# Optimization experiments

Measured on AMD Instinct MI355X. Metric: run time of the kernel, lower is better.

Reference implementation:

```python
import jax, jax.numpy as jnp
import numpy as np
from jax.ops import segment_sum, segment_max

B, NPG, EPG = 2048, 32, 64          # graphs per drug, nodes/graph, edges/graph
N, E = B * NPG, B * EPG
FIN, EIN = 70, 6
HID, H, C = 128, 2, 64              # hidd_dim, conv heads, head_out_feats
NBLK, NCLASS = 4, 2
CAH, CAD = 8, 128                   # co-attention heads, dim_head


def _elu(x):
    return jnp.where(x > 0, x, jnp.expm1(x))


def _ln_graph(x, batch, w, b):
    # PyG LayerNorm(mode='graph'): normalize over all nodes+channels of each graph.
    cnt = jnp.float32(NPG * x.shape[1])  # all graphs have NPG nodes
    mean = segment_sum(x.sum(-1), batch, num_segments=B) / cnt
    xc = x - mean[batch][:, None]
    var = segment_sum((xc * xc).sum(-1), batch, num_segments=B) / cnt
    return xc * jax.lax.rsqrt(var + 1e-5)[batch][:, None] * w + b


def _ln(x, w, b):
    mu = x.mean(-1, keepdims=True)
    v = ((x - mu) ** 2).mean(-1, keepdims=True)
    return (x - mu) * jax.lax.rsqrt(v + 1e-5) * w + b


def _tconv(x, src, dst, ea, Wq, bq, Wk, bk, Wv, bv, We, Ws, bs):
    # PyG TransformerConv: edge-attention gather -> softmax over incoming edges -> scatter.
    q = (x @ Wq + bq).reshape(-1, H, C)
    k = (x @ Wk + bk).reshape(-1, H, C)
    v = (x @ Wv + bv).reshape(-1, H, C)
    e = (ea @ We).reshape(-1, H, C)
    kj = k[src] + e                                   # [E,H,C]
    a = (q[dst] * kj).sum(-1) * (C ** -0.5)           # [E,H]
    amax = segment_max(a, dst, num_segments=N)
    a = jnp.exp(a - amax[dst])
    a = a / (segment_sum(a, dst, num_segments=N)[dst] + 1e-16)
    out = segment_sum((v[src] + e) * a[:, :, None], dst, num_segments=N)
    return out.reshape(-1, H * C) + x @ Ws + bs       # root/skip connection


def _pool(x, src, dst, ea, batch, ebatch, w_rel, b_rel, w_root, W_re, b_re):
    # SAGPooling(min_score=-1): GraphConv score, per-graph softmax, all nodes kept,
    # then score-weighted global_add_pool; edge_attr pooled per graph and merged.
    agg = segment_sum(x[src], dst, num_segments=N)    # GraphConv 'add' aggregation
    score = agg @ w_rel + b_rel + x @ w_root          # [N]
    smax = segment_max(score, batch, num_segments=B)
    sexp = jnp.exp(score - smax[batch])
    score = sexp / (segment_sum(sexp, batch, num_segments=B)[batch] + 1e-16)
    g = segment_sum(x * score[:, None], batch, num_segments=B)      # [B,HID]
    ge = _elu(segment_sum(ea, ebatch, num_segments=B) @ W_re + b_re)
    g = g * ge
    return g / jnp.maximum(jnp.linalg.norm(g, axis=1, keepdims=True), 1e-12)


def _coattn(qx, kvx, lw, lb, Wq, Wkv, Wo):
    qx = _ln(qx, lw, lb)
    kvx = _ln(kvx, lw, lb)
    b, n = qx.shape[0], qx.shape[1]
    q = (qx @ Wq).reshape(b, n, CAH, CAD).transpose(0, 2, 1, 3)
    k, v = jnp.split(kvx @ Wkv, 2, axis=-1)
    k = k.reshape(b, n, CAH, CAD).transpose(0, 2, 1, 3)
    v = v.reshape(b, n, CAH, CAD).transpose(0, 2, 1, 3)
    attn = jax.nn.softmax(jnp.einsum('bhnd,bhmd->bhnm', q, k) * (CAD ** -0.5), axis=-1)
    o = jnp.einsum('bhnm,bhmd->bhnd', attn, v).transpose(0, 2, 1, 3).reshape(b, n, CAH * CAD)
    return o @ Wo


def setup_inputs() -> dict:
    key = jax.random.key(0)
    ks = iter(jax.random.split(key, 64))

    def nrm(shape, fan):
        return jax.random.normal(next(ks), shape, jnp.float32) * (fan ** -0.5)

    inp = {}
    inp['x1'] = jax.random.normal(next(ks), (N, FIN), jnp.float32)
    inp['x2'] = jax.random.normal(next(ks), (N, FIN), jnp.float32)
    inp['ea1'] = jax.random.normal(next(ks), (E, EIN), jnp.float32)
    inp['ea2'] = jax.random.normal(next(ks), (E, EIN), jnp.float32)
    inp['W_node'] = nrm((FIN, HID), FIN); inp['b_node'] = jnp.zeros((HID,), jnp.float32)
    inp['W_edge'] = nrm((EIN, 64), EIN); inp['b_edge'] = jnp.zeros((64,), jnp.float32)
    inp['ln0_w'] = jnp.ones((HID,), jnp.float32); inp['ln0_b'] = jnp.zeros((HID,), jnp.float32)
    inp['Wq'] = nrm((NBLK, 2, HID, HID), HID); inp['bq'] = jnp.zeros((NBLK, 2, HID), jnp.float32)
    inp['Wk'] = nrm((NBLK, 2, HID, HID), HID); inp['bk'] = jnp.zeros((NBLK, 2, HID), jnp.float32)
    inp['Wv'] = nrm((NBLK, 2, HID, HID), HID); inp['bv'] = jnp.zeros((NBLK, 2, HID), jnp.float32)
    inp['We'] = nrm((NBLK, 2, 64, HID), 64)
    inp['Ws'] = nrm((NBLK, 2, HID, HID), HID); inp['bs'] = jnp.zeros((NBLK, 2, HID), jnp.float32)
    inp['Wup'] = nrm((NBLK, 2, 64, 64), 64); inp['bup'] = jnp.zeros((NBLK, 2, 64), jnp.float32)
    inp['lnw'] = jnp.ones((NBLK, 2, HID), jnp.float32); inp['lnb'] = jnp.zeros((NBLK, 2, HID), jnp.float32)
    inp['w_rel'] = nrm((HID,), HID); inp['b_rel'] = jnp.zeros((), jnp.float32)
    inp['w_root'] = nrm((HID,), HID)
    inp['W_re'] = nrm((64, HID), 64); inp['b_re'] = jnp.zeros((HID,), jnp.float32)
    inp['ca_lw'] = jnp.ones((HID,), jnp.float32); inp['ca_lb'] = jnp.zeros((HID,), jnp.float32)
    inp['Wq_ca'] = nrm((HID, CAH * CAD), HID)
    inp['Wkv_ca'] = nrm((HID, 2 * CAH * CAD), HID)
    inp['Wo_ca'] = nrm((CAH * CAD, HID), CAH * CAD)
    inp['W_merge'] = nrm((NBLK * NBLK, NCLASS), NBLK * NBLK)
    inp['b_merge'] = jnp.zeros((NCLASS,), jnp.float32)
    off = jnp.repeat(jnp.arange(B, dtype=jnp.int32) * NPG, EPG)
    inp['edge_index1'] = jax.random.randint(next(ks), (2, E), 0, NPG, jnp.int32) + off[None, :]
    inp['edge_index2'] = jax.random.randint(next(ks), (2, E), 0, NPG, jnp.int32) + off[None, :]
    inp['batch1'] = jnp.repeat(jnp.arange(B, dtype=jnp.int32), NPG)
    inp['batch2'] = jnp.repeat(jnp.arange(B, dtype=jnp.int32), NPG)
    inp['ebatch1'] = jnp.repeat(jnp.arange(B, dtype=jnp.int32), EPG)
    inp['ebatch2'] = jnp.repeat(jnp.arange(B, dtype=jnp.int32), EPG)
    return inp


def reference(x1, x2, ea1, ea2, W_node, b_node, W_edge, b_edge, ln0_w, ln0_b,
              Wq, bq, Wk, bk, Wv, bv, We, Ws, bs, Wup, bup, lnw, lnb,
              w_rel, b_rel, w_root, W_re, b_re, ca_lw, ca_lb, Wq_ca, Wkv_ca, Wo_ca,
              W_merge, b_merge, edge_index1, edge_index2, batch1, batch2, ebatch1, ebatch2):
    s1, d1 = edge_index1[0], edge_index1[1]
    s2, d2 = edge_index2[0], edge_index2[1]
    x1 = _elu(_ln_graph(x1 @ W_node + b_node, batch1, ln0_w, ln0_b))
    x2 = _elu(_ln_graph(x2 @ W_node + b_node, batch2, ln0_w, ln0_b))
    ea1 = _elu(ea1 @ W_edge + b_edge)
    ea2 = _elu(ea2 @ W_edge + b_edge)

    def block(i, x, ea, src, dst, batch):
        x = _tconv(x, src, dst, ea, Wq[i, 0], bq[i, 0], Wk[i, 0], bk[i, 0],
                   Wv[i, 0], bv[i, 0], We[i, 0], Ws[i, 0], bs[i, 0])
        x = _elu(_ln_graph(x, batch, lnw[i, 0], lnb[i, 0]))
        ea = _elu(ea @ Wup[i, 0] + bup[i, 0])
        x = _tconv(x, src, dst, ea, Wq[i, 1], bq[i, 1], Wk[i, 1], bk[i, 1],
                   Wv[i, 1], bv[i, 1], We[i, 1], Ws[i, 1], bs[i, 1])
        ea_next = ea @ Wup[i, 1] + bup[i, 1]
        x = _elu(_ln_graph(x, batch, lnw[i, 1], lnb[i, 1]))
        return x, _elu(ea_next)

    hs, ts = [], []
    for i in range(NBLK):
        x1, ea1 = block(i, x1, ea1, s1, d1, batch1)
        x2, ea2 = block(i, x2, ea2, s2, d2, batch2)
        hs.append(_pool(x1, s1, d1, ea1, batch1, ebatch1, w_rel, b_rel, w_root, W_re, b_re))
        ts.append(_pool(x2, s2, d2, ea2, batch2, ebatch2, w_rel, b_rel, w_root, W_re, b_re))
    rh = jnp.stack(hs, 1)  # [B, NBLK, HID]
    rt = jnp.stack(ts, 1)
    ha = _coattn(rh, rt, ca_lw, ca_lb, Wq_ca, Wkv_ca, Wo_ca)
    ta = _coattn(rt, rh, ca_lw, ca_lb, Wq_ca, Wkv_ca, Wo_ca)
    m = jnp.einsum('bnd,bmd->bnm', ha, ta).reshape(ha.shape[0], NBLK * NBLK)
    return jax.nn.softmax(m @ W_merge + b_merge, axis=-1)
```

## Files before the change

### kernel.cpp

```cpp
#include <hip/hip_runtime.h>
#include <cstddef>
#include <cstdint>

#define NGRAPH 2048
#define NPG    32
#define EPG    64
#define NNODE  (NGRAPH*NPG)
#define NEDGE  (NGRAPH*EPG)
#define FINDIM 70
#define EINDIM 6
#define HID    128
#define NBLK   4
#define CAH    8
#define CAD    128
#define ES     68
#define XS     132

typedef __attribute__((ext_vector_type(8))) short bf16x8_t;
typedef __attribute__((ext_vector_type(4))) float f32x4;
typedef unsigned short ushortb;

#define MF3(accv, Ah_, Al_, Bh_, Bl_)                                          \
  accv = __builtin_amdgcn_mfma_f32_16x16x32_bf16(Ah_, Bh_, accv, 0, 0, 0);     \
  accv = __builtin_amdgcn_mfma_f32_16x16x32_bf16(Ah_, Bl_, accv, 0, 0, 0);     \
  accv = __builtin_amdgcn_mfma_f32_16x16x32_bf16(Al_, Bh_, accv, 0, 0, 0);

__device__ inline void split8(const float* p, bf16x8_t& h, bf16x8_t& l) {
  float4 v0 = *(const float4*)p, v1 = *(const float4*)(p + 4);
  float vv[8] = {v0.x, v0.y, v0.z, v0.w, v1.x, v1.y, v1.z, v1.w};
#pragma unroll
  for (int j = 0; j < 8; j++) {
    unsigned u = __builtin_bit_cast(unsigned, vv[j]);
    h[j] = (short)(u >> 16);
    float r = vv[j] - __builtin_bit_cast(float, u & 0xFFFF0000u);
    l[j] = (short)(__builtin_bit_cast(unsigned, r) >> 16);
  }
}

template<bool BIAS, bool ELU>
__global__ __launch_bounds__(256) void gemm_kernel(
    const float* __restrict__ A, const float* __restrict__ W,
    const float* __restrict__ bias, float* __restrict__ C,
    int M, int K, int Nc) {
  __shared__ float As[8][64];
  __shared__ float Bs[8][65];
  const int bm = blockIdx.y * 64, bn = blockIdx.x * 64;
  const int tid = threadIdx.x;
  const int tr = tid >> 4, tc = tid & 15;
  float acc[4][4];
#pragma unroll
  for (int i = 0; i < 4; i++)
#pragma unroll
    for (int j = 0; j < 4; j++) acc[i][j] = 0.f;
  for (int k0 = 0; k0 < K; k0 += 8) {
#pragma unroll
    for (int l = 0; l < 2; l++) {
      int idx = tid + l * 256;
      int r = idx >> 3, c = idx & 7;
      As[c][r] = (k0 + c < K) ? A[(size_t)(bm + r) * K + k0 + c] : 0.f;
      int rw = idx >> 6, cw = idx & 63;
      Bs[rw][cw] = (k0 + rw < K) ? W[(size_t)(k0 + rw) * Nc + bn + cw] : 0.f;
    }
    __syncthreads();
#pragma unroll
    for (int kk = 0; kk < 8; kk++) {
      float a_[4], w_[4];
#pragma unroll
      for (int i = 0; i < 4; i++) a_[i] = As[kk][tr * 4 + i];
#pragma unroll
// ... 122 lines not shown
  for (int m = 0; m < 2; m++)
#pragma unroll
    for (int n = 0; n < 4; n++) {
      int col = bn + wc * 64 + n * 16 + l16;
#pragma unroll
      for (int r = 0; r < 4; r++) {
        int row = bm + wr * 32 + m * 16 + lk * 4 + r;
        C[(size_t)row * N + col] = acc[m][n][r];
      }
    }
}

static void run_mf8(const float* A, const ushortb* Wh, const ushortb* Wl,
                    float* C, int M, int K, int N, hipStream_t st) {
  dim3 grid(N / 128, M / 128), block(512);
  gemm_mfma8_kernel<<<grid, block, 0, st>>>(A, Wh, Wl, C, M, K, N);
}

__global__ void ln_graph_elu_kernel(const float* __restrict__ in, float* __restrict__ out,
                                    const float* __restrict__ w, const float* __restrict__ b) {
  const int g = blockIdx.x, t = threadIdx.x;
  const float* xg = in + (size_t)g * NPG * HID;
  float* og = out + (size_t)g * NPG * HID;
  float vals[16];
  float s = 0.f, ss = 0.f;
#pragma unroll
  for (int i = 0; i < 16; i++) {
    float v = xg[t + i * 256];
    vals[i] = v; s += v; ss += v * v;
  }
  __shared__ float ws0[4], ws1[4];
  for (int off = 32; off > 0; off >>= 1) { s += __shfl_down(s, off); ss += __shfl_down(ss, off); }
  int wid = t >> 6, lane = t & 63;
  if (lane == 0) { ws0[wid] = s; ws1[wid] = ss; }
  __syncthreads();
  if (t == 0) {
    float S = 0.f, SS = 0.f;
    for (int i = 0; i < 4; i++) { S += ws0[i]; SS += ws1[i]; }
    float mean = S / 4096.f;
    float var = SS / 4096.f - mean * mean;
    ws0[0] = mean; ws1[0] = rsqrtf(var + 1e-5f);
  }
  __syncthreads();
  float mean = ws0[0], inv = ws1[0];
#pragma unroll
  for (int i = 0; i < 16; i++) {
    int idx = t + i * 256;
    int ch = idx & 127;
    float y = (vals[i] - mean) * inv * w[ch] + b[ch];
    og[idx] = y > 0.f ? y : expm1f(y);
  }
}

template<bool POOL>
__global__ __launch_bounds__(256, 4) void mega_kernel(
    float* __restrict__ xb, float* __restrict__ ea,
    const ushortb* __restrict__ Wqkvh, const ushortb* __restrict__ Wqkvl,
    const ushortb* __restrict__ Wsh, const ushortb* __restrict__ Wsl,
    const ushortb* __restrict__ WeTh, const ushortb* __restrict__ WeTl,
    const ushortb* __restrict__ Wuph, const ushortb* __restrict__ Wupl,
    const float* __restrict__ bqkv_, const float* __restrict__ bs_,
    const float* __restrict__ bup_, const float* __restrict__ lnw_,
    const float* __restrict__ lnb_,
    const float* __restrict__ w_rel, const float* __restrict__ b_rel,
    const float* __restrict__ w_root, const float* __restrict__ W_re,
    const float* __restrict__ b_re, float* __restrict__ outp, int blk,
    const int* __restrict__ src, const int* __restrict__ dst) {
  const int g = blockIdx.x, t = threadIdx.x;
  const int lane = t & 63, w = t >> 6, l16 = lane & 15, lk = lane >> 4;
  __shared__ float el[EPG * ES];
  __shared__ float qs2[NPG * ES];
  __shared__ float ks2[NPG * ES];
  __shared__ unsigned char lists[NPG * EPG];
  __shared__ int deg_[NPG];
  __shared__ int sl[EPG], dl[EPG];
  __shared__ float alE[128];
  __shared__ float red0[NPG], red1[NPG];

  if (t < EPG) { sl[t] = src[g * EPG + t] - g * NPG; dl[t] = dst[g * EPG + t] - g * NPG; }
  if (t < NPG) {
    int c = 0;
    for (int e = 0; e < EPG; e++)
      if (dl[e] == t) lists[t * EPG + (c++)] = (unsigned char)e;
    deg_[t] = c;
  }

  bf16x8_t xh[2][4], xL[2][4];
#pragma unroll
  for (int m = 0; m < 2; m++)
#pragma unroll
    for (int kc = 0; kc < 4; kc++)
      split8(xb + ((size_t)g * NPG + m * 16 + l16) * HID + kc * 32 + lk * 8,
             xh[m][kc], xL[m][kc]);
  const float* eag = ea + ((size_t)g * EPG + w * 16 + l16) * 64;

  float accH0[8], accH1[8];
#pragma unroll
  for (int c = 0; c < 8; c++) { accH0[c] = 0.f; accH1[c] = 0.f; }

  auto proj = [&](int baseN, float* dstL) {
    f32x4 pa0 = (f32x4)0.f, pa1 = (f32x4)0.f;
#pragma unroll
    for (int kc = 0; kc < 4; kc++) {
      size_t o = (size_t)(baseN + w * 16 + l16) * HID + kc * 32 + lk * 8;
      bf16x8_t bh = *(const bf16x8_t*)(Wqkvh + o);
      bf16x8_t bl = *(const bf16x8_t*)(Wqkvl + o);
      MF3(pa0, xh[0][kc], xL[0][kc], bh, bl);
      MF3(pa1, xh[1][kc], xL[1][kc], bh, bl);
    }
    float bv = bqkv_[baseN + w * 16 + l16];
#pragma unroll
    for (int r = 0; r < 4; r++) {
      dstL[(lk * 4 + r) * ES + w * 16 + l16] = pa0[r] + bv;
      dstL[(16 + lk * 4 + r) * ES + w * 16 + l16] = pa1[r] + bv;
    }
  };

  auto head = [&](const int h, float (&acc8)[8]) {
    {
      bf16x8_t ea0h, ea0l, ea1h, ea1l;
      split8(eag + lk * 8, ea0h, ea0l);
      split8(eag + 32 + lk * 8, ea1h, ea1l);
#pragma unroll 1
      for (int n = 0; n < 4; n++) {
        f32x4 acc = (f32x4)0.f;
        size_t o0 = (size_t)(h * 64 + n * 16 + l16) * 64 + lk * 8;
        bf16x8_t bh0 = *(const bf16x8_t*)(WeTh + o0);
        bf16x8_t bl0 = *(const bf16x8_t*)(WeTl + o0);
        MF3(acc, ea0h, ea0l, bh0, bl0);
        bf16x8_t bh1 = *(const bf16x8_t*)(WeTh + o0 + 32);
        bf16x8_t bl1 = *(const bf16x8_t*)(WeTl + o0 + 32);
        MF3(acc, ea1h, ea1l, bh1, bl1);
#pragma unroll
        for (int r = 0; r < 4; r++)
          el[(w * 16 + lk * 4 + r) * ES + n * 16 + l16] = acc[r];
      }
    }
    proj(h * 64, qs2);
    proj(128 + h * 64, ks2);
    __syncthreads();
    {
      const int e2 = t >> 2, part = t & 3;
      const float* qp = qs2 + dl[e2] * ES + part * 16;
      const float* kp = ks2 + sl[e2] * ES + part * 16;
      const float* ep = el + e2 * ES + part * 16;
      float s = 0.f;
#pragma unroll
      for (int c = 0; c < 16; c += 4) {
        float4 qv = *(const float4*)(qp + c);
        float4 kv = *(const float4*)(kp + c);
        float4 ev = *(const float4*)(ep + c);
        s += qv.x * (kv.x + ev.x) + qv.y * (kv.y + ev.y) +
             qv.z * (kv.z + ev.z) + qv.w * (kv.w + ev.w);
      }
      s += __shfl_xor(s, 1);
      s += __shfl_xor(s, 2);
      if (part == 0) alE[e2] = s * 0.125f;
    }
    __syncthreads();
    {
      const int n = t >> 3, part = t & 7;
      float m = -1e30f;
#pragma unroll 1
      for (int i = 0; i < 8; i++) {
        int e2 = part * 8 + i;
        if (dl[e2] == n) m = fmaxf(m, alE[e2]);
      }
      m = fmaxf(m, __shfl_xor(m, 1));
      m = fmaxf(m, __shfl_xor(m, 2));
      m = fmaxf(m, __shfl_xor(m, 4));
      float su = 0.f;
#pragma unroll 1
      for (int i = 0; i < 8; i++) {
        int e2 = part * 8 + i;
        if (dl[e2] == n) su += expf(alE[e2] - m);
      }
      su += __shfl_xor(su, 1);
      su += __shfl_xor(su, 2);
      su += __shfl_xor(su, 4);
      if (part == 0) { red0[n] = m; red1[n] = su; }
    }
    __syncthreads();
    if (t < EPG) {
      int n = dl[t];
      alE[t] = expf(alE[t] - red0[n]) / (red1[n] + 1e-16f);
    }
    f32x4 va0 = (f32x4)0.f, va1 = (f32x4)0.f;
#pragma unroll
    for (int kc = 0; kc < 4; kc++) {
      size_t o = (size_t)(256 + h * 64 + w * 16 + l16) * HID + kc * 32 + lk * 8;
      bf16x8_t bh = *(const bf16x8_t*)(Wqkvh + o);
      bf16x8_t bl = *(const bf16x8_t*)(Wqkvl + o);
      MF3(va0, xh[0][kc], xL[0][kc], bh, bl);
      MF3(va1, xh[1][kc], xL[1][kc], bh, bl);
    }
    float bv = bqkv_[256 + h * 64 + w * 16 + l16];
    __syncthreads();
#pragma unroll
    for (int r = 0; r < 4; r++) {
      ks2[(lk * 4 + r) * ES + w * 16 + l16] = va0[r] + bv;
      ks2[(16 + lk * 4 + r) * ES + w * 16 + l16] = va1[r] + bv;
    }
    __syncthreads();
    {
      const int n = t >> 3, cg = t & 7;
      const int dg = deg_[n];
      for (int i = 0; i < dg; i++) {
        const int e2 = lists[n * EPG + i];
        const float a = alE[e2];
        const float* vp = ks2 + sl[e2] * ES + cg * 8;
        const float* ep = el + e2 * ES + cg * 8;
        float4 v0 = *(const float4*)vp, v1 = *(const float4*)(vp + 4);
        float4 e0 = *(const float4*)ep, e1 = *(const float4*)(ep + 4);
        acc8[0] += a * (v0.x + e0.x); acc8[1] += a * (v0.y + e0.y);
        acc8[2] += a * (v0.z + e0.z); acc8[3] += a * (v0.w + e0.w);
        acc8[4] += a * (v1.x + e1.x); acc8[5] += a * (v1.y + e1.y);
        acc8[6] += a * (v1.z + e1.z); acc8[7] += a * (v1.w + e1.w);
      }
    }
    __syncthreads();
  };

  head(0, accH0);
  head(1, accH1);

  {
#pragma unroll
    for (int n = 0; n < 2; n++) {
      f32x4 sa0 = (f32x4)0.f, sa1 = (f32x4)0.f;
#pragma unroll
      for (int kc = 0; kc < 4; kc++) {
        size_t o = (size_t)(w * 32 + n * 16 + l16) * HID + kc * 32 + lk * 8;
        bf16x8_t bh = *(const bf16x8_t*)(Wsh + o);
        bf16x8_t bl = *(const bf16x8_t*)(Wsl + o);
        MF3(sa0, xh[0][kc], xL[0][kc], bh, bl);
        MF3(sa1, xh[1][kc], xL[1][kc], bh, bl);
      }
      int col = w * 32 + n * 16 + l16;
      float bv = bs_[col];
#pragma unroll
      for (int r = 0; r < 4; r++) {
        el[(lk * 4 + r) * XS + col] = sa0[r] + bv;
        el[(16 + lk * 4 + r) * XS + col] = sa1[r] + bv;
      }
    }
  }
  f32x4 ua[4];
  {
    bf16x8_t ea0h, ea0l, ea1h, ea1l;
    split8(eag + lk * 8, ea0h, ea0l);
    split8(eag + 32 + lk * 8, ea1h, ea1l);
#pragma unroll
    for (int n = 0; n < 4; n++) {
      f32x4 acc = (f32x4)0.f;
      size_t o0 = (size_t)(n * 16 + l16) * 64 + lk * 8;
      bf16x8_t bh0 = *(const bf16x8_t*)(Wuph + o0);
      bf16x8_t bl0 = *(const bf16x8_t*)(Wupl + o0);
      MF3(acc, ea0h, ea0l, bh0, bl0);
      bf16x8_t bh1 = *(const bf16x8_t*)(Wuph + o0 + 32);
      bf16x8_t bl1 = *(const bf16x8_t*)(Wupl + o0 + 32);
      MF3(acc, ea1h, ea1l, bh1, bl1);
      int col = n * 16 + l16;
      float bv = bup_[col];
#pragma unroll
      for (int r = 0; r < 4; r++) {
        float y = acc[r] + bv;
        y = y > 0.f ? y : expm1f(y);
        ua[n][r] = y;
        ea[((size_t)g * EPG + w * 16 + lk * 4 + r) * 64 + col] = y;
      }
    }
  }
  __syncthreads();
  {
    const int n = t >> 3, cg = t & 7;
    float v16[16];
#pragma unroll
    for (int c = 0; c < 8; c++) {
      v16[c] = accH0[c] + el[n * XS + cg * 8 + c];
      v16[8 + c] = accH1[c] + el[n * XS + 64 + cg * 8 + c];
    }
    float s = 0.f, ss = 0.f;
#pragma unroll
    for (int j = 0; j < 16; j++) { s += v16[j]; ss += v16[j] * v16[j]; }
    for (int o2 = 32; o2 > 0; o2 >>= 1) { s += __shfl_down(s, o2); ss += __shfl_down(ss, o2); }
    if (lane == 0) { red0[w] = s; red1[w] = ss; }
    __syncthreads();
    if (t == 0) {
      float S = red0[0] + red0[1] + red0[2] + red0[3];
      float SS = red1[0] + red1[1] + red1[2] + red1[3];
      float mean = S / 4096.f;
      float var = SS / 4096.f - mean * mean;
      red0[0] = mean; red1[0] = rsqrtf(var + 1e-5f);
    }
    __syncthreads();
    float mean = red0[0], inv = red1[0];
    float* xg = xb + (size_t)g * NPG * HID;
#pragma unroll
    for (int hh = 0; hh < 2; hh++)
#pragma unroll
      for (int c = 0; c < 8; c++) {
        int col = hh * 64 + cg * 8 + c;
        float y = (v16[hh * 8 + c] - mean) * inv * lnw_[col] + lnb_[col];
        y = y > 0.f ? y : expm1f(y);
        xg[n * HID + col] = y;
        el[n * XS + col] = y;
      }
  }

  if constexpr (POOL) {
    __syncthreads();
    {
#pragma unroll
      for (int n = 0; n < 4; n++) {
        float s = ua[n][0] + ua[n][1] + ua[n][2] + ua[n][3];
        s += __shfl_xor(s, 16);
        s += __shfl_xor(s, 32);
        if (lk == 0) qs2[w * 64 + n * 16 + l16] = s;
      }
      const int n = t >> 3, part = t & 7;
      float s = 0.f;
      for (int c = part * 16; c < part * 16 + 16; c++)
        s += el[n * XS + c] * w_root[c];
      const int dg = deg_[n];
      for (int i = 0; i < dg; i++) {
        int sn = sl[lists[n * EPG + i]];
        for (int c = part * 16; c < part * 16 + 16; c++)
          s += el[sn * XS + c] * w_rel[c];
      }
      s += __shfl_xor(s, 1);
      s += __shfl_xor(s, 2);
      s += __shfl_xor(s, 4);
      if (part == 0) alE[n] = s + b_rel[0];
    }
    __syncthreads();
    if (t < 64)
      alE[64 + t] = qs2[t] + qs2[64 + t] + qs2[128 + t] + qs2[192 + t];
    if (t >= 128 && t < 160) {
      int n = t - 128;
      float sc = alE[n];
      float m = sc;
      for (int o2 = 1; o2 <= 16; o2 <<= 1) m = fmaxf(m, __shfl_xor(m, o2));
      float e = expf(sc - m);
      float su = e;
      for (int o2 = 1; o2 <= 16; o2 <<= 1) su += __shfl_xor(su, o2);
      alE[n] = e / (su + 1e-16f);
    }
    __syncthreads();
    if (t < HID) {
      const int ch = t;
      float gv = 0.f;
      for (int n = 0; n < NPG; n++) gv += alE[n] * el[n * XS + ch];
      float s2 = b_re[ch];
      for (int k2 = 0; k2 < 64; k2++) s2 += alE[64 + k2] * W_re[k2 * HID + ch];
      s2 = s2 > 0.f ? s2 : expm1f(s2);
      float gl = gv * s2;
      qs2[256 + ch] = gl;
      float sq = gl * gl;
      for (int o2 = 32; o2 > 0; o2 >>= 1) sq += __shfl_down(sq, o2);
      if (lane == 0) red0[w] = sq;
    }
    __syncthreads();
    if (t == 0) red1[0] = fmaxf(sqrtf(red0[0] + red0[1]), 1e-12f);
    __syncthreads();
    if (t < HID)
      outp[((size_t)g * NBLK + blk) * HID + t] = qs2[256 + t] / red1[0];
  }
}

__global__ void ln_row_kernel(const float* __restrict__ in, float* __restrict__ out,
                              const float* __restrict__ w, const float* __restrict__ b) {
  const int r = blockIdx.x, t = threadIdx.x;
  float v = in[(size_t)r * HID + t];
  float s = v, ss = v * v;
  for (int off = 32; off > 0; off >>= 1) { s += __shfl_down(s, off); ss += __shfl_down(ss, off); }
  __shared__ float s0[2], s1[2];
  if ((t & 63) == 0) { s0[t >> 6] = s; s1[t >> 6] = ss; }
  __syncthreads();
  float S = s0[0] + s0[1], SS = s1[0] + s1[1];
  float mean = S / 128.f, var = SS / 128.f - mean * mean;
  out[(size_t)r * HID + t] = (v - mean) * rsqrtf(var + 1e-5f) * w[t] + b[t];
}

__global__ void coattn_kernel(const float* __restrict__ qb, const float* __restrict__ kvb,
                              float* __restrict__ ob) {
  const int bh = blockIdx.x, b = bh >> 3, h = bh & 7, t = threadIdx.x;
  __shared__ float attn[4][4];
  __shared__ float red[64];
  const int pair = t >> 2, part = t & 3;
  const int n = pair >> 2, m = pair & 3;
  const float* qp = qb + ((size_t)(b * 4 + n) * (CAH * CAD)) + h * CAD;
  const float* kp = kvb + ((size_t)(b * 4 + m) * (2 * CAH * CAD)) + h * CAD;
  float s = 0.f;
  for (int d = part * 32; d < part * 32 + 32; d++) s += qp[d] * kp[d];
  red[t] = s;
  __syncthreads();
  if (t < 16) {
    float sc = (red[t * 4] + red[t * 4 + 1] + red[t * 4 + 2] + red[t * 4 + 3]) * 0.08838834764831845f;
    attn[t >> 2][t & 3] = sc;
  }
  __syncthreads();
  if (t < 4) {
    float m_ = -1e30f;
    for (int j = 0; j < 4; j++) m_ = fmaxf(m_, attn[t][j]);
    float ex[4], su = 0.f;
    for (int j = 0; j < 4; j++) { ex[j] = expf(attn[t][j] - m_); su += ex[j]; }
    for (int j = 0; j < 4; j++) attn[t][j] = ex[j] / su;
  }
  __syncthreads();
  for (int i = t; i < 512; i += 64) {
    int n2 = i >> 7, d = i & 127;
    float acc = 0.f;
    for (int m2 = 0; m2 < 4; m2++)
      acc += attn[n2][m2] * kvb[((size_t)(b * 4 + m2) * (2 * CAH * CAD)) + CAH * CAD + h * CAD + d];
    ob[((size_t)(b * 4 + n2) * (CAH * CAD)) + h * CAD + d] = acc;
  }
}

__global__ void final_kernel(const float* __restrict__ ha, const float* __restrict__ ta,
// ... 68 lines not shown
    off += ((elems * 4 + 255) & ~(size_t)255);
    return r;
  };
  auto allocb = [&](size_t elems) {
    ushortb* r = (ushortb*)(base + off);
    off += ((elems * 2 + 255) & ~(size_t)255);
    return r;
  };
  float* xb  = alloc((size_t)NNODE * HID);
  float* ea  = alloc((size_t)NEDGE * 64);
  float* big = alloc((size_t)8192 * 2048);
  float* hs  = alloc((size_t)NGRAPH * NBLK * HID);
  float* ts  = alloc((size_t)NGRAPH * NBLK * HID);
  float* rhn = alloc((size_t)NGRAPH * NBLK * HID);
  float* rtn = alloc((size_t)NGRAPH * NBLK * HID);
  float* hab = alloc((size_t)NGRAPH * NBLK * HID);
  float* tab = alloc((size_t)NGRAPH * NBLK * HID);
  ushortb* Wqkvh = allocb((size_t)8 * 384 * 128); ushortb* Wqkvl = allocb((size_t)8 * 384 * 128);
  ushortb* Wsh = allocb(8 * 16384);  ushortb* Wsl = allocb(8 * 16384);
  ushortb* Wuph = allocb(8 * 4096);  ushortb* Wupl = allocb(8 * 4096);
  ushortb* WeTh = allocb(8 * 8192);  ushortb* WeTl = allocb(8 * 8192);
  ushortb* Wqcah = allocb(131072);   ushortb* Wqcal = allocb(131072);
  ushortb* Wkvh = allocb(262144);    ushortb* Wkvl = allocb(262144);
  ushortb* Woh = allocb(131072);     ushortb* Wol = allocb(131072);
  float* bqkv = alloc(8 * 384);
  if (off > ws_size) return;

  float* qc  = xb;
  float* kvc = big;
  float* oc  = ea;

  auto convw = [&](const float* s, ushortb* h, ushortb* l, int K, int N, int B,
                   int dstN, int nOff) {
    int tot = B * K * N;
    convw_kernel<<<(tot + 255) / 256, 256, 0, stream>>>(s, h, l, K, N, tot, dstN, nOff);
  };
  convw(Wq, Wqkvh, Wqkvl, 128, 128, 8, 384, 0);
  convw(Wk, Wqkvh, Wqkvl, 128, 128, 8, 384, 128);
  convw(Wv, Wqkvh, Wqkvl, 128, 128, 8, 384, 256);
  convw(Wskip, Wsh, Wsl, 128, 128, 8, 128, 0);
  convw(Wup, Wuph, Wupl, 64, 64, 8, 64, 0);
  convw(We, WeTh, WeTl, 64, 128, 8, 128, 0);
  convw(Wq_ca, Wqcah, Wqcal, 128, 1024, 1, 1024, 0);
  convw(Wkv_ca, Wkvh, Wkvl, 128, 2048, 1, 2048, 0);
  convw(Wo_ca, Woh, Wol, 1024, 128, 1, 128, 0);
  bcat_kernel<<<(8 * 384 + 255) / 256, 256, 0, stream>>>(bq, bk, bv, bqkv);

  for (int d2 = 0; d2 < 2; ++d2) {
    const int* src = ei[d2];
    const int* dst = ei[d2] + NEDGE;
    run_gemm(xin[d2], W_node, b_node, xb, NNODE, FINDIM, HID, false, stream);
    ln_graph_elu_kernel<<<NGRAPH, 256, 0, stream>>>(xb, xb, ln0_w, ln0_b);
    run_gemm(eain[d2], W_edge, b_edge, ea, NEDGE, EINDIM, 64, true, stream);
    float* outp = d2 == 0 ? hs : ts;
    for (int i = 0; i < NBLK; ++i) {
      int pi0 = i * 2, pi1 = i * 2 + 1;
      mega_kernel<false><<<NGRAPH, 256, 0, stream>>>(
          xb, ea,
          Wqkvh + (size_t)pi0 * 49152, Wqkvl + (size_t)pi0 * 49152,
          Wsh + (size_t)pi0 * 16384, Wsl + (size_t)pi0 * 16384,
          WeTh + (size_t)pi0 * 8192, WeTl + (size_t)pi0 * 8192,
          Wuph + (size_t)pi0 * 4096, Wupl + (size_t)pi0 * 4096,
          bqkv + pi0 * 384, bs + pi0 * 128, bup + pi0 * 64,
          lnw + pi0 * 128, lnb + pi0 * 128,
          w_rel, b_rel, w_root, W_re, b_re, nullptr, 0, src, dst);
      mega_kernel<true><<<NGRAPH, 256, 0, stream>>>(
          xb, ea,
          Wqkvh + (size_t)pi1 * 49152, Wqkvl + (size_t)pi1 * 49152,
          Wsh + (size_t)pi1 * 16384, Wsl + (size_t)pi1 * 16384,
          WeTh + (size_t)pi1 * 8192, WeTl + (size_t)pi1 * 8192,
          Wuph + (size_t)pi1 * 4096, Wupl + (size_t)pi1 * 4096,
          bqkv + pi1 * 384, bs + pi1 * 128, bup + pi1 * 64,
          lnw + pi1 * 128, lnb + pi1 * 128,
          w_rel, b_rel, w_root, W_re, b_re, outp, i, src, dst);
    }
  }

  ln_row_kernel<<<NGRAPH * NBLK, 128, 0, stream>>>(hs, rhn, ca_lw, ca_lb);
  ln_row_kernel<<<NGRAPH * NBLK, 128, 0, stream>>>(ts, rtn, ca_lw, ca_lb);
  run_mf8(rhn, Wqcah, Wqcal, qc, NGRAPH * NBLK, 128, 1024, stream);
  run_mf8(rtn, Wkvh, Wkvl, kvc, NGRAPH * NBLK, 128, 2048, stream);
  coattn_kernel<<<NGRAPH * CAH, 64, 0, stream>>>(qc, kvc, oc);
  run_mf8(oc, Woh, Wol, hab, NGRAPH * NBLK, 1024, 128, stream);
  run_mf8(rtn, Wqcah, Wqcal, qc, NGRAPH * NBLK, 128, 1024, stream);
  run_mf8(rhn, Wkvh, Wkvl, kvc, NGRAPH * NBLK, 128, 2048, stream);
  coattn_kernel<<<NGRAPH * CAH, 64, 0, stream>>>(qc, kvc, oc);
  run_mf8(oc, Woh, Wol, tab, NGRAPH * NBLK, 1024, 128, stream);

  final_kernel<<<NGRAPH, 64, 0, stream>>>(hab, tab, W_merge, b_merge, out);
}
```

Baseline: 3.239 ms.

## Fuse all eight conv layers into one persistent per-graph kernel with on-chip state

Replaces eight separate per-layer launches with one kernel per drug that loops over all conv layers. Node features and edge attributes stay in shared memory and registers between layers instead of going through global memory. This removes launch overhead and the global traffic to write and re-read x and ea each layer. The cost is a longer kernel body, some shared-memory aliasing (qks reused for edge attributes), and possible register pressure that could lower occupancy.

```diff
diff --git a/kernel.cpp b/kernel.cpp
--- a/kernel.cpp
+++ b/kernel.cpp
@@ -15,6 +15,7 @@
 #define CAD    128
 #define ES     68
 #define XS     132
+#define TS     66
 
 typedef __attribute__((ext_vector_type(8))) short bf16x8_t;
 typedef __attribute__((ext_vector_type(4))) float f32x4;
@@ -243,30 +244,30 @@
   }
 }
 
-template<bool POOL>
 __global__ __launch_bounds__(256, 4) void mega_kernel(
-    float* __restrict__ xb, float* __restrict__ ea,
-    const ushortb* __restrict__ Wqkvh, const ushortb* __restrict__ Wqkvl,
-    const ushortb* __restrict__ Wsh, const ushortb* __restrict__ Wsl,
-    const ushortb* __restrict__ WeTh, const ushortb* __restrict__ WeTl,
-    const ushortb* __restrict__ Wuph, const ushortb* __restrict__ Wupl,
-    const float* __restrict__ bqkv_, const float* __restrict__ bs_,
-    const float* __restrict__ bup_, const float* __restrict__ lnw_,
-    const float* __restrict__ lnb_,
+    const float* __restrict__ xb, const float* __restrict__ ea,
+    const ushortb* __restrict__ Wqkvh_, const ushortb* __restrict__ Wqkvl_,
+    const ushortb* __restrict__ Wsh_, const ushortb* __restrict__ Wsl_,
+    const ushortb* __restrict__ WeTh_, const ushortb* __restrict__ WeTl_,
+    const ushortb* __restrict__ Wuph_, const ushortb* __restrict__ Wupl_,
+    const float* __restrict__ bqkvA, const float* __restrict__ bsA,
+    const float* __restrict__ bupA, const float* __restrict__ lnwA,
+    const float* __restrict__ lnbA,
     const float* __restrict__ w_rel, const float* __restrict__ b_rel,
     const float* __restrict__ w_root, const float* __restrict__ W_re,
-    const float* __restrict__ b_re, float* __restrict__ outp, int blk,
+    const float* __restrict__ b_re, float* __restrict__ outp,
     const int* __restrict__ src, const int* __restrict__ dst) {
   const int g = blockIdx.x, t = threadIdx.x;
   const int lane = t & 63, w = t >> 6, l16 = lane & 15, lk = lane >> 4;
   __shared__ float el[EPG * ES];
-  __shared__ float qs2[NPG * ES];
-  __shared__ float ks2[NPG * ES];
+  __shared__ float qks[2 * NPG * ES];
   __shared__ unsigned char lists[NPG * EPG];
   __shared__ int deg_[NPG];
   __shared__ int sl[EPG], dl[EPG];
   __shared__ float alE[128];
   __shared__ float red0[NPG], red1[NPG];
+  float* qs2 = qks;
+  float* ks2 = qks + NPG * ES;
 
   if (t < EPG) { sl[t] = src[g * EPG + t] - g * NPG; dl[t] = dst[g * EPG + t] - g * NPG; }
   if (t < NPG) {
@@ -283,279 +284,299 @@
     for (int kc = 0; kc < 4; kc++)
       split8(xb + ((size_t)g * NPG + m * 16 + l16) * HID + kc * 32 + lk * 8,
              xh[m][kc], xL[m][kc]);
-  const float* eag = ea + ((size_t)g * EPG + w * 16 + l16) * 64;
-
-  float accH0[8], accH1[8];
-#pragma unroll
-  for (int c = 0; c < 8; c++) { accH0[c] = 0.f; accH1[c] = 0.f; }
-
-  auto proj = [&](int baseN, float* dstL) {
-    f32x4 pa0 = (f32x4)0.f, pa1 = (f32x4)0.f;
-#pragma unroll
-    for (int kc = 0; kc < 4; kc++) {
-      size_t o = (size_t)(baseN + w * 16 + l16) * HID + kc * 32 + lk * 8;
-      bf16x8_t bh = *(const bf16x8_t*)(Wqkvh + o);
-      bf16x8_t bl = *(const bf16x8_t*)(Wqkvl + o);
-      MF3(pa0, xh[0][kc], xL[0][kc], bh, bl);
-      MF3(pa1, xh[1][kc], xL[1][kc], bh, bl);
-    }
-    float bv = bqkv_[baseN + w * 16 + l16];
-#pragma unroll
-    for (int r = 0; r < 4; r++) {
-      dstL[(lk * 4 + r) * ES + w * 16 + l16] = pa0[r] + bv;
-      dstL[(16 + lk * 4 + r) * ES + w * 16 + l16] = pa1[r] + bv;
-    }
-  };
-
-  auto head = [&](const int h, float (&acc8)[8]) {
+  bf16x8_t eah[2], eaL[2];
+  {
+    const float* eag = ea + ((size_t)g * EPG + w * 16 + l16) * 64;
+    split8(eag + lk * 8, eah[0], eaL[0]);
+    split8(eag + 32 + lk * 8, eah[1], eaL[1]);
+  }
+
+  for (int pi = 0; pi < 8; ++pi) {
+    const ushortb* Wqkvh = Wqkvh_ + (size_t)pi * 49152;
+    const ushortb* Wqkvl = Wqkvl_ + (size_t)pi * 49152;
+    const ushortb* Wsh = Wsh_ + (size_t)pi * 16384;
+    const ushortb* Wsl = Wsl_ + (size_t)pi * 16384;
+    const ushortb* WeTh = WeTh_ + (size_t)pi * 8192;
+    const ushortb* WeTl = WeTl_ + (size_t)pi * 8192;
+    const ushortb* Wuph = Wuph_ + (size_t)pi * 4096;
+    const ushortb* Wupl = Wupl_ + (size_t)pi * 4096;
+    const float* bqkv_ = bqkvA + pi * 384;
+    const float* bs_ = bsA + pi * 128;
+    const float* bup_ = bupA + pi * 64;
+    const float* lnw_ = lnwA + pi * 128;
+    const float* lnb_ = lnbA + pi * 128;
+
+    float accH0[8], accH1[8];
+#pragma unroll
+    for (int c = 0; c < 8; c++) { accH0[c] = 0.f; accH1[c] = 0.f; }
+
+    auto proj = [&](int baseN, float* dstL) {
+      f32x4 pa0 = (f32x4)0.f, pa1 = (f32x4)0.f;
+#pragma unroll
+      for (int kc = 0; kc < 4; kc++) {
+        size_t o = (size_t)(baseN + w * 16 + l16) * HID + kc * 32 + lk * 8;
+        bf16x8_t bh = *(const bf16x8_t*)(Wqkvh + o);
+        bf16x8_t bl = *(const bf16x8_t*)(Wqkvl + o);
+        MF3(pa0, xh[0][kc], xL[0][kc], bh, bl);
+        MF3(pa1, xh[1][kc], xL[1][kc], bh, bl);
+      }
+      float bv = bqkv_[baseN + w * 16 + l16];
+#pragma unroll
+      for (int r = 0; r < 4; r++) {
+        dstL[(lk * 4 + r) * ES + w * 16 + l16] = pa0[r] + bv;
+        dstL[(16 + lk * 4 + r) * ES + w * 16 + l16] = pa1[r] + bv;
+      }
+    };
+
+    auto head = [&](const int h, float (&acc8)[8]) {
+      {
+#pragma unroll 1
+        for (int n = 0; n < 4; n++) {
+          f32x4 acc = (f32x4)0.f;
+          size_t o0 = (size_t)(h * 64 + n * 16 + l16) * 64 + lk * 8;
+          bf16x8_t bh0 = *(const bf16x8_t*)(WeTh + o0);
+          bf16x8_t bl0 = *(const bf16x8_t*)(WeTl + o0);
+          MF3(acc, eah[0], eaL[0], bh0, bl0);
+          bf16x8_t bh1 = *(const bf16x8_t*)(WeTh + o0 + 32);
+          bf16x8_t bl1 = *(const bf16x8_t*)(WeTl + o0 + 32);
+          MF3(acc, eah[1], eaL[1], bh1, bl1);
+#pragma unroll
+          for (int r = 0; r < 4; r++)
+            el[(w * 16 + lk * 4 + r) * ES + n * 16 + l16] = acc[r];
+        }
+      }
+      proj(h * 64, qs2);
+      proj(128 + h * 64, ks2);
+      __syncthreads();
+      {
+        const int e2 = t >> 2, part = t & 3;
+        const float* qp = qs2 + dl[e2] * ES + part * 16;
+        const float* kp = ks2 + sl[e2] * ES + part * 16;
+        const float* ep = el + e2 * ES + part * 16;
+        float s = 0.f;
+#pragma unroll
+        for (int c = 0; c < 16; c += 4) {
+          float4 qv = *(const float4*)(qp + c);
+          float4 kv = *(const float4*)(kp + c);
+          float4 ev = *(const float4*)(ep + c);
+          s += qv.x * (kv.x + ev.x) + qv.y * (kv.y + ev.y) +
+               qv.z * (kv.z + ev.z) + qv.w * (kv.w + ev.w);
+        }
+        s += __shfl_xor(s, 1);
+        s += __shfl_xor(s, 2);
+        if (part == 0) alE[e2] = s * 0.125f;
+      }
+      __syncthreads();
+      {
+        const int n = t >> 3, part = t & 7;
+        float m = -1e30f;
+#pragma unroll 1
+        for (int i = 0; i < 8; i++) {
+          int e2 = part * 8 + i;
+          if (dl[e2] == n) m = fmaxf(m, alE[e2]);
+        }
+        m = fmaxf(m, __shfl_xor(m, 1));
+        m = fmaxf(m, __shfl_xor(m, 2));
+        m = fmaxf(m, __shfl_xor(m, 4));
+        float su = 0.f;
+#pragma unroll 1
+        for (int i = 0; i < 8; i++) {
+          int e2 = part * 8 + i;
+          if (dl[e2] == n) su += expf(alE[e2] - m);
+        }
+        su += __shfl_xor(su, 1);
+        su += __shfl_xor(su, 2);
+        su += __shfl_xor(su, 4);
+        if (part == 0) { red0[n] = m; red1[n] = su; }
+      }
+      __syncthreads();
+      if (t < EPG) {
+        int n = dl[t];
+        alE[t] = expf(alE[t] - red0[n]) / (red1[n] + 1e-16f);
+      }
+      f32x4 va0 = (f32x4)0.f, va1 = (f32x4)0.f;
+#pragma unroll
+      for (int kc = 0; kc < 4; kc++) {
+        size_t o = (size_t)(256 + h * 64 + w * 16 + l16) * HID + kc * 32 + lk * 8;
+        bf16x8_t bh = *(const bf16x8_t*)(Wqkvh + o);
+        bf16x8_t bl = *(const bf16x8_t*)(Wqkvl + o);
+        MF3(va0, xh[0][kc], xL[0][kc], bh, bl);
+        MF3(va1, xh[1][kc], xL[1][kc], bh, bl);
+      }
+      float bv = bqkv_[256 + h * 64 + w * 16 + l16];
+      __syncthreads();
+#pragma unroll
+      for (int r = 0; r < 4; r++) {
+        ks2[(lk * 4 + r) * ES + w * 16 + l16] = va0[r] + bv;
+        ks2[(16 + lk * 4 + r) * ES + w * 16 + l16] = va1[r] + bv;
+      }
+      __syncthreads();
+      {
+        const int n = t >> 3, cg = t & 7;
+        const int dg = deg_[n];
+        for (int i = 0; i < dg; i++) {
+          const int e2 = lists[n * EPG + i];
+          const float a = alE[e2];
+          const float* vp = ks2 + sl[e2] * ES + cg * 8;
+          const float* ep = el + e2 * ES + cg * 8;
+          float4 v0 = *(const float4*)vp, v1 = *(const float4*)(vp + 4);
+          float4 e0 = *(const float4*)ep, e1 = *(const float4*)(ep + 4);
+          acc8[0] += a * (v0.x + e0.x); acc8[1] += a * (v0.y + e0.y);
+          acc8[2] += a * (v0.z + e0.z); acc8[3] += a * (v0.w + e0.w);
+          acc8[4] += a * (v1.x + e1.x); acc8[5] += a * (v1.y + e1.y);
+          acc8[6] += a * (v1.z + e1.z); acc8[7] += a * (v1.w + e1.w);
+        }
+      }
+      __syncthreads();
+    };
+
+    head(0, accH0);
+    head(1, accH1);
+
     {
-      bf16x8_t ea0h, ea0l, ea1h, ea1l;
-      split8(eag + lk * 8, ea0h, ea0l);
-      split8(eag + 32 + lk * 8, ea1h, ea1l);
-#pragma unroll 1
+#pragma unroll
+      for (int n = 0; n < 2; n++) {
+        f32x4 sa0 = (f32x4)0.f, sa1 = (f32x4)0.f;
+#pragma unroll
+        for (int kc = 0; kc < 4; kc++) {
+          size_t o = (size_t)(w * 32 + n * 16 + l16) * HID + kc * 32 + lk * 8;
+          bf16x8_t bh = *(const bf16x8_t*)(Wsh + o);
+          bf16x8_t bl = *(const bf16x8_t*)(Wsl + o);
+          MF3(sa0, xh[0][kc], xL[0][kc], bh, bl);
+          MF3(sa1, xh[1][kc], xL[1][kc], bh, bl);
+        }
+        int col = w * 32 + n * 16 + l16;
+        float bv = bs_[col];
+#pragma unroll
+        for (int r = 0; r < 4; r++) {
+          el[(lk * 4 + r) * XS + col] = sa0[r] + bv;
+          el[(16 + lk * 4 + r) * XS + col] = sa1[r] + bv;
+        }
+      }
+    }
+    {
+#pragma unroll
       for (int n = 0; n < 4; n++) {
         f32x4 acc = (f32x4)0.f;
-        size_t o0 = (size_t)(h * 64 + n * 16 + l16) * 64 + lk * 8;
-        bf16x8_t bh0 = *(const bf16x8_t*)(WeTh + o0);
-        bf16x8_t bl0 = *(const bf16x8_t*)(WeTl + o0);
-        MF3(acc, ea0h, ea0l, bh0, bl0);
-        bf16x8_t bh1 = *(const bf16x8_t*)(WeTh + o0 + 32);
-        bf16x8_t bl1 = *(const bf16x8_t*)(WeTl + o0 + 32);
-        MF3(acc, ea1h, ea1l, bh1, bl1);
-#pragma unroll
-        for (int r = 0; r < 4; r++)
-          el[(w * 16 + lk * 4 + r) * ES + n * 16 + l16] = acc[r];
-      }
-    }
-    proj(h * 64, qs2);
-    proj(128 + h * 64, ks2);
-    __syncthreads();
-    {
-      const int e2 = t >> 2, part = t & 3;
-      const float* qp = qs2 + dl[e2] * ES + part * 16;
-      const float* kp = ks2 + sl[e2] * ES + part * 16;
-      const float* ep = el + e2 * ES + part * 16;
-      float s = 0.f;
-#pragma unroll
-      for (int c = 0; c < 16; c += 4) {
-        float4 qv = *(const float4*)(qp + c);
-        float4 kv = *(const float4*)(kp + c);
-        float4 ev = *(const float4*)(ep + c);
-        s += qv.x * (kv.x + ev.x) + qv.y * (kv.y + ev.y) +
-             qv.z * (kv.z + ev.z) + qv.w * (kv.w + ev.w);
-      }
-      s += __shfl_xor(s, 1);
-      s += __shfl_xor(s, 2);
-      if (part == 0) alE[e2] = s * 0.125f;
-    }
-    __syncthreads();
-    {
-      const int n = t >> 3, part = t & 7;
-      float m = -1e30f;
-#pragma unroll 1
-      for (int i = 0; i < 8; i++) {
-        int e2 = part * 8 + i;
-        if (dl[e2] == n) m = fmaxf(m, alE[e2]);
-      }
-      m = fmaxf(m, __shfl_xor(m, 1));
-      m = fmaxf(m, __shfl_xor(m, 2));
-      m = fmaxf(m, __shfl_xor(m, 4));
-      float su = 0.f;
-#pragma unroll 1
-      for (int i = 0; i < 8; i++) {
-        int e2 = part * 8 + i;
-        if (dl[e2] == n) su += expf(alE[e2] - m);
-      }
-      su += __shfl_xor(su, 1);
-      su += __shfl_xor(su, 2);
-      su += __shfl_xor(su, 4);
-      if (part == 0) { red0[n] = m; red1[n] = su; }
-    }
-    __syncthreads();
-    if (t < EPG) {
-      int n = dl[t];
-      alE[t] = expf(alE[t] - red0[n]) / (red1[n] + 1e-16f);
-    }
-    f32x4 va0 = (f32x4)0.f, va1 = (f32x4)0.f;
-#pragma unroll
-    for (int kc = 0; kc < 4; kc++) {
-      size_t o = (size_t)(256 + h * 64 + w * 16 + l16) * HID + kc * 32 + lk * 8;
-      bf16x8_t bh = *(const bf16x8_t*)(Wqkvh + o);
-      bf16x8_t bl = *(const bf16x8_t*)(Wqkvl + o);
-      MF3(va0, xh[0][kc], xL[0][kc], bh, bl);
-      MF3(va1, xh[1][kc], xL[1][kc], bh, bl);
-    }
-    float bv = bqkv_[256 + h * 64 + w * 16 + l16];
-    __syncthreads();
-#pragma unroll
-    for (int r = 0; r < 4; r++) {
-      ks2[(lk * 4 + r) * ES + w * 16 + l16] = va0[r] + bv;
-      ks2[(16 + lk * 4 + r) * ES + w * 16 + l16] = va1[r] + bv;
+        size_t o0 = (size_t)(n * 16 + l16) * 64 + lk * 8;
+        bf16x8_t bh0 = *(const bf16x8_t*)(Wuph + o0);
+        bf16x8_t bl0 = *(const bf16x8_t*)(Wupl + o0);
+        MF3(acc, eah[0], eaL[0], bh0, bl0);
+        bf16x8_t bh1 = *(const bf16x8_t*)(Wuph + o0 + 32);
+        bf16x8_t bl1 = *(const bf16x8_t*)(Wupl + o0 + 32);
+        MF3(acc, eah[1], eaL[1], bh1, bl1);
+        int col = n * 16 + l16;
+        float bv = bup_[col];
+#pragma unroll
+        for (int r = 0; r < 4; r++) {
+          float y = acc[r] + bv;
+          y = y > 0.f ? y : expm1f(y);
+          qks[(w * 16 + lk * 4 + r) * TS + col] = y;
+        }
+      }
     }
     __syncthreads();
     {
       const int n = t >> 3, cg = t & 7;
-      const int dg = deg_[n];
-      for (int i = 0; i < dg; i++) {
-        const int e2 = lists[n * EPG + i];
-        const float a = alE[e2];
-        const float* vp = ks2 + sl[e2] * ES + cg * 8;
-        const float* ep = el + e2 * ES + cg * 8;
-        float4 v0 = *(const float4*)vp, v1 = *(const float4*)(vp + 4);
-        float4 e0 = *(const float4*)ep, e1 = *(const float4*)(ep + 4);
-        acc8[0] += a * (v0.x + e0.x); acc8[1] += a * (v0.y + e0.y);
-        acc8[2] += a * (v0.z + e0.z); acc8[3] += a * (v0.w + e0.w);
-        acc8[4] += a * (v1.x + e1.x); acc8[5] += a * (v1.y + e1.y);
-        acc8[6] += a * (v1.z + e1.z); acc8[7] += a * (v1.w + e1.w);
-      }
-    }
-    __syncthreads();
-  };
-
-  head(0, accH0);
-  head(1, accH1);
-
-  {
-#pragma unroll
-    for (int n = 0; n < 2; n++) {
-      f32x4 sa0 = (f32x4)0.f, sa1 = (f32x4)0.f;
-#pragma unroll
-      for (int kc = 0; kc < 4; kc++) {
-        size_t o = (size_t)(w * 32 + n * 16 + l16) * HID + kc * 32 + lk * 8;
-        bf16x8_t bh = *(const bf16x8_t*)(Wsh + o);
-        bf16x8_t bl = *(const bf16x8_t*)(Wsl + o);
-        MF3(sa0, xh[0][kc], xL[0][kc], bh, bl);
-        MF3(sa1, xh[1][kc], xL[1][kc], bh, bl);
-      }
-      int col = w * 32 + n * 16 + l16;
-      float bv = bs_[col];
-#pragma unroll
-      for (int r = 0; r < 4; r++) {
-        el[(lk * 4 + r) * XS + col] = sa0[r] + bv;
-        el[(16 + lk * 4 + r) * XS + col] = sa1[r] + bv;
-      }
-    }
-  }
-  f32x4 ua[4];
-  {
-    bf16x8_t ea0h, ea0l, ea1h, ea1l;
-    split8(eag + lk * 8, ea0h, ea0l);
-    split8(eag + 32 + lk * 8, ea1h, ea1l);
-#pragma unroll
-    for (int n = 0; n < 4; n++) {
-      f32x4 acc = (f32x4)0.f;
-      size_t o0 = (size_t)(n * 16 + l16) * 64 + lk * 8;
-      bf16x8_t bh0 = *(const bf16x8_t*)(Wuph + o0);
-      bf16x8_t bl0 = *(const bf16x8_t*)(Wupl + o0);
-      MF3(acc, ea0h, ea0l, bh0, bl0);
-      bf16x8_t bh1 = *(const bf16x8_t*)(Wuph + o0 + 32);
-      bf16x8_t bl1 = *(const bf16x8_t*)(Wupl + o0 + 32);
-      MF3(acc, ea1h, ea1l, bh1, bl1);
-      int col = n * 16 + l16;
-      float bv = bup_[col];
-#pragma unroll
-      for (int r = 0; r < 4; r++) {
-        float y = acc[r] + bv;
-        y = y > 0.f ? y : expm1f(y);
-        ua[n][r] = y;
-        ea[((size_t)g * EPG + w * 16 + lk * 4 + r) * 64 + col] = y;
-      }
-    }
-  }
-  __syncthreads();
-  {
-    const int n = t >> 3, cg = t & 7;
-    float v16[16];
-#pragma unroll
-    for (int c = 0; c < 8; c++) {
-      v16[c] = accH0[c] + el[n * XS + cg * 8 + c];
-      v16[8 + c] = accH1[c] + el[n * XS + 64 + cg * 8 + c];
-    }
-    float s = 0.f, ss = 0.f;
-#pragma unroll
-    for (int j = 0; j < 16; j++) { s += v16[j]; ss += v16[j] * v16[j]; }
-    for (int o2 = 32; o2 > 0; o2 >>= 1) { s += __shfl_down(s, o2); ss += __shfl_down(ss, o2); }
-    if (lane == 0) { red0[w] = s; red1[w] = ss; }
-    __syncthreads();
-    if (t == 0) {
-      float S = red0[0] + red0[1] + red0[2] + red0[3];
-      float SS = red1[0] + red1[1] + red1[2] + red1[3];
-      float mean = S / 4096.f;
-      float var = SS / 4096.f - mean * mean;
-      red0[0] = mean; red1[0] = rsqrtf(var + 1e-5f);
-    }
-    __syncthreads();
-    float mean = red0[0], inv = red1[0];
-    float* xg = xb + (size_t)g * NPG * HID;
-#pragma unroll
-    for (int hh = 0; hh < 2; hh++)
+      float v16[16];
 #pragma unroll
       for (int c = 0; c < 8; c++) {
-        int col = hh * 64 + cg * 8 + c;
-        float y = (v16[hh * 8 + c] - mean) * inv * lnw_[col] + lnb_[col];
-        y = y > 0.f ? y : expm1f(y);
-        xg[n * HID + col] = y;
-        el[n * XS + col] = y;
-      }
-  }
-
-  if constexpr (POOL) {
-    __syncthreads();
-    {
-#pragma unroll
-      for (int n = 0; n < 4; n++) {
-        float s = ua[n][0] + ua[n][1] + ua[n][2] + ua[n][3];
-        s += __shfl_xor(s, 16);
-        s += __shfl_xor(s, 32);
-        if (lk == 0) qs2[w * 64 + n * 16 + l16] = s;
-      }
-      const int n = t >> 3, part = t & 7;
-      float s = 0.f;
-      for (int c = part * 16; c < part * 16 + 16; c++)
-        s += el[n * XS + c] * w_root[c];
-      const int dg = deg_[n];
-      for (int i = 0; i < dg; i++) {
-        int sn = sl[lists[n * EPG + i]];
+        v16[c] = accH0[c] + el[n * XS + cg * 8 + c];
+        v16[8 + c] = accH1[c] + el[n * XS + 64 + cg * 8 + c];
+      }
+      float s = 0.f, ss = 0.f;
+#pragma unroll
+      for (int j = 0; j < 16; j++) { s += v16[j]; ss += v16[j] * v16[j]; }
+      for (int o2 = 32; o2 > 0; o2 >>= 1) { s += __shfl_down(s, o2); ss += __shfl_down(ss, o2); }
+      if (lane == 0) { red0[w] = s; red1[w] = ss; }
+      __syncthreads();
+      if (t == 0) {
+        float S = red0[0] + red0[1] + red0[2] + red0[3];
+        float SS = red1[0] + red1[1] + red1[2] + red1[3];
+        float mean = S / 4096.f;
+        float var = SS / 4096.f - mean * mean;
+        red0[0] = mean; red1[0] = rsqrtf(var + 1e-5f);
+      }
+      __syncthreads();
+      float mean = red0[0], inv = red1[0];
+#pragma unroll
+      for (int hh = 0; hh < 2; hh++)
+#pragma unroll
+        for (int c = 0; c < 8; c++) {
+          int col = hh * 64 + cg * 8 + c;
+          float y = (v16[hh * 8 + c] - mean) * inv * lnw_[col] + lnb_[col];
+          y = y > 0.f ? y : expm1f(y);
+          el[n * XS + col] = y;
+        }
+    }
+
+    if (pi & 1) {
+      __syncthreads();
+      {
+        const int n = t >> 3, part = t & 7;
+        float s = 0.f;
         for (int c = part * 16; c < part * 16 + 16; c++)
-          s += el[sn * XS + c] * w_rel[c];
-      }
-      s += __shfl_xor(s, 1);
-      s += __shfl_xor(s, 2);
-      s += __shfl_xor(s, 4);
-      if (part == 0) alE[n] = s + b_rel[0];
-    }
-    __syncthreads();
-    if (t < 64)
-      alE[64 + t] = qs2[t] + qs2[64 + t] + qs2[128 + t] + qs2[192 + t];
-    if (t >= 128 && t < 160) {
-      int n = t - 128;
-      float sc = alE[n];
-      float m = sc;
-      for (int o2 = 1; o2 <= 16; o2 <<= 1) m = fmaxf(m, __shfl_xor(m, o2));
-      float e = expf(sc - m);
-      float su = e;
-      for (int o2 = 1; o2 <= 16; o2 <<= 1) su += __shfl_xor(su, o2);
-      alE[n] = e / (su + 1e-16f);
-    }
-    __syncthreads();
-    if (t < HID) {
-      const int ch = t;
-      float gv = 0.f;
-      for (int n = 0; n < NPG; n++) gv += alE[n] * el[n * XS + ch];
-      float s2 = b_re[ch];
-      for (int k2 = 0; k2 < 64; k2++) s2 += alE[64 + k2] * W_re[k2 * HID + ch];
-      s2 = s2 > 0.f ? s2 : expm1f(s2);
-      float gl = gv * s2;
-      qs2[256 + ch] = gl;
-      float sq = gl * gl;
-      for (int o2 = 32; o2 > 0; o2 >>= 1) sq += __shfl_down(sq, o2);
-      if (lane == 0) red0[w] = sq;
-    }
-    __syncthreads();
-    if (t == 0) red1[0] = fmaxf(sqrtf(red0[0] + red0[1]), 1e-12f);
-    __syncthreads();
-    if (t < HID)
-      outp[((size_t)g * NBLK + blk) * HID + t] = qs2[256 + t] / red1[0];
+          s += el[n * XS + c] * w_root[c];
+        const int dg = deg_[n];
+        for (int i = 0; i < dg; i++) {
+          int sn = sl[lists[n * EPG + i]];
+          for (int c = part * 16; c < part * 16 + 16; c++)
+            s += el[sn * XS + c] * w_rel[c];
+        }
+        s += __shfl_xor(s, 1);
+        s += __shfl_xor(s, 2);
+        s += __shfl_xor(s, 4);
+        if (part == 0) alE[n] = s + b_rel[0];
+      }
+      if (t < 64) {
+        float s = 0.f;
+#pragma unroll 1
+        for (int r = 0; r < EPG; r++) s += qks[r * TS + t];
+        alE[64 + t] = s;
+      }
+      __syncthreads();
+      if (t >= 128 && t < 160) {
+        int n = t - 128;
+        float sc = alE[n];
+        float m = sc;
+        for (int o2 = 1; o2 <= 16; o2 <<= 1) m = fmaxf(m, __shfl_xor(m, o2));
+        float e = expf(sc - m);
+        float su = e;
+        for (int o2 = 1; o2 <= 16; o2 <<= 1) su += __shfl_xor(su, o2);
+        alE[n] = e / (su + 1e-16f);
+      }
+      __syncthreads();
+      if (t < HID) {
+        const int ch = t;
+        float gv = 0.f;
+        for (int n = 0; n < NPG; n++) gv += alE[n] * el[n * XS + ch];
+        float s2 = b_re[ch];
+        for (int k2 = 0; k2 < 64; k2++) s2 += alE[64 + k2] * W_re[k2 * HID + ch];
+        s2 = s2 > 0.f ? s2 : expm1f(s2);
+        float gl = gv * s2;
+        el[4224 + ch] = gl;
+        float sq = gl * gl;
+        for (int o2 = 32; o2 > 0; o2 >>= 1) sq += __shfl_down(sq, o2);
+        if (lane == 0) red0[w] = sq;
+      }
+      __syncthreads();
+      if (t == 0) red1[0] = fmaxf(sqrtf(red0[0] + red0[1]), 1e-12f);
+      __syncthreads();
+      if (t < HID)
+        outp[((size_t)g * NBLK + (pi >> 1)) * HID + t] = el[4224 + t] / red1[0];
+    }
+
+    if (pi < 7) {
+      __syncthreads();
+#pragma unroll
+      for (int m = 0; m < 2; m++)
+#pragma unroll
+        for (int kc = 0; kc < 4; kc++)
+          split8(&el[(m * 16 + l16) * XS + kc * 32 + lk * 8], xh[m][kc], xL[m][kc]);
+      split8(&qks[(w * 16 + l16) * TS + lk * 8], eah[0], eaL[0]);
+      split8(&qks[(w * 16 + l16) * TS + 32 + lk * 8], eah[1], eaL[1]);
+      __syncthreads();
+    }
   }
 }
 
@@ -730,28 +751,10 @@
     run_gemm(xin[d2], W_node, b_node, xb, NNODE, FINDIM, HID, false, stream);
     ln_graph_elu_kernel<<<NGRAPH, 256, 0, stream>>>(xb, xb, ln0_w, ln0_b);
     run_gemm(eain[d2], W_edge, b_edge, ea, NEDGE, EINDIM, 64, true, stream);
-    float* outp = d2 == 0 ? hs : ts;
-    for (int i = 0; i < NBLK; ++i) {
-      int pi0 = i * 2, pi1 = i * 2 + 1;
-      mega_kernel<false><<<NGRAPH, 256, 0, stream>>>(
-          xb, ea,
-          Wqkvh + (size_t)pi0 * 49152, Wqkvl + (size_t)pi0 * 49152,
-          Wsh + (size_t)pi0 * 16384, Wsl + (size_t)pi0 * 16384,
-          WeTh + (size_t)pi0 * 8192, WeTl + (size_t)pi0 * 8192,
-          Wuph + (size_t)pi0 * 4096, Wupl + (size_t)pi0 * 4096,
-          bqkv + pi0 * 384, bs + pi0 * 128, bup + pi0 * 64,
-          lnw + pi0 * 128, lnb + pi0 * 128,
-          w_rel, b_rel, w_root, W_re, b_re, nullptr, 0, src, dst);
-      mega_kernel<true><<<NGRAPH, 256, 0, stream>>>(
-          xb, ea,
-          Wqkvh + (size_t)pi1 * 49152, Wqkvl + (size_t)pi1 * 49152,
-          Wsh + (size_t)pi1 * 16384, Wsl + (size_t)pi1 * 16384,
-          WeTh + (size_t)pi1 * 8192, WeTl + (size_t)pi1 * 8192,
-          Wuph + (size_t)pi1 * 4096, Wupl + (size_t)pi1 * 4096,
-          bqkv + pi1 * 384, bs + pi1 * 128, bup + pi1 * 64,
-          lnw + pi1 * 128, lnb + pi1 * 128,
-          w_rel, b_rel, w_root, W_re, b_re, outp, i, src, dst);
-    }
+    mega_kernel<<<NGRAPH, 256, 0, stream>>>(
+        xb, ea, Wqkvh, Wqkvl, Wsh, Wsl, WeTh, WeTl, Wuph, Wupl,
+        bqkv, bs, bup, lnw, lnb,
+        w_rel, b_rel, w_root, W_re, b_re, d2 == 0 ? hs : ts, src, dst);
   }
 
   ln_row_kernel<<<NGRAPH * NBLK, 128, 0, stream>>>(hs, rhn, ca_lw, ca_lb);
```

After: 4.398 ms. +35.8%, slower.
